# Optimization experiments

Measured on AMD Instinct MI355X. Metric: run time of the kernel, lower is better.

## Reference

```python
import jax, jax.numpy as jnp
import numpy as np

K_KNN = 20
TC = 3  # taylor_channel
N_TERMS = 20  # trivariate polynomial terms up to order 3
CHANNELS = [(6, 32), (32, 64), (64, 128), (128, 256)]


def _knn_indices(xyz, k):
    sq = jnp.sum(xyz * xyz, axis=1)  # B x N
    d2 = sq[:, :, None] + sq[:, None, :] - 2.0 * jnp.einsum('bci,bcj->bij', xyz, xyz)
    _, idx = jax.lax.top_k(-d2, k)
    return idx


def _group(feat, idx):
    # feat: B x C x N, idx: B x N x K -> B x C x N x K
    return jax.vmap(lambda f, i: f[:, i])(feat, idx)


def _taylor_terms(g):
    X, Y, Z = g[:, 0], g[:, 1], g[:, 2]
    one = jnp.ones_like(X)
    terms = [one, X, Y, Z, X * Y, X * Z, Y * Z, X * X, Y * Y, Z * Z,
             X * X * Y, X * X * Z, X * Y * Y, Y * Y * Z, X * Z * Z, Y * Z * Z,
             X * Y * Z, X * X * X, Y * Y * Y, Z * Z * Z]
    return jnp.stack(terms, axis=1)


def _spider_conv(feat, idx, terms, w1, b1, w2, b2):
    # feat: B x C x N; w1: tc x 20; w2: out x (C*tc) x K
    B, C, N = feat.shape
    g = _group(feat, idx)  # B x C x N x K
    taylor = jnp.einsum('btnk,ot->bonk', terms, w1) + b1[None, :, None, None]
    g = (g[:, :, None, :, :] * taylor[:, None, :, :, :]).reshape(B, C * TC, N, g.shape[-1])
    out = jnp.einsum('bcnk,ock->bon', g, w2) + b2[None, :, None]
    return jax.nn.relu(out)


def _forward(pc, params):
    # pc: B x N x 6
    pcT = jnp.transpose(pc, (0, 2, 1))
    xyz = pcT[:, 0:3, :]
    idx = _knn_indices(xyz, K_KNN)  # B x N x K
    grouped_xyz = _group(xyz, idx)
    grouped_pc = grouped_xyz - xyz[:, :, :, None]  # relative coords
    terms = _taylor_terms(grouped_pc)
    feat = pcT
    feats = []
    for l in range(4):
        w1, b1, w2, b2 = params[l]
        feat = _spider_conv(feat, idx, terms, w1, b1, w2, b2)
        feats.append(feat)
    cat = jnp.concatenate(feats, axis=1)
    top2, _ = jax.lax.top_k(cat, 2)  # topk over point dim (last axis)
    return top2.reshape(cat.shape[0], -1)  # B x 960


def setup_inputs() -> dict:
    key = jax.random.key(0)
    keys = jax.random.split(key, 1 + 16)
    B, N = 4, 2048
    inp = {'pc': jax.random.normal(keys[0], (B, N, 6), dtype=jnp.float32)}
    ki = 1
    for l, (cin, cout) in enumerate(CHANNELS):
        inp[f'w1_{l}'] = jax.random.normal(keys[ki], (TC, N_TERMS), dtype=jnp.float32) * 0.1; ki += 1
        inp[f'b1_{l}'] = jax.random.normal(keys[ki], (TC,), dtype=jnp.float32) * 0.01; ki += 1
        inp[f'w2_{l}'] = jax.random.normal(keys[ki], (cout, cin * TC, K_KNN), dtype=jnp.float32) * (1.0 / np.sqrt(cin * TC * K_KNN)); ki += 1
        inp[f'b2_{l}'] = jax.random.normal(keys[ki], (cout,), dtype=jnp.float32) * 0.01; ki += 1
    return inp


def reference(pc, w1_0, b1_0, w2_0, b2_0, w1_1, b1_1, w2_1, b2_1,
              w1_2, b1_2, w2_2, b2_2, w1_3, b1_3, w2_3, b2_3):
    params = [(w1_0, b1_0, w2_0, b2_0), (w1_1, b1_1, w2_1, b2_1),
              (w1_2, b1_2, w2_2, b2_2), (w1_3, b1_3, w2_3, b2_3)]
    return _forward(pc, params)
```

## Files before the change

### kernel.cpp

```cpp
#include <hip/hip_runtime.h>
#include <math.h>

#define BB 4
#define NN 2048
#define KNN 20

typedef _Float16 f16x8 __attribute__((ext_vector_type(8)));
typedef _Float16 f16x4 __attribute__((ext_vector_type(4)));
typedef _Float16 f16x2 __attribute__((ext_vector_type(2)));
typedef float f32x4 __attribute__((ext_vector_type(4)));

#define DPP_STEP(CTRL, RMASK)                                                   \
    {                                                                           \
        unsigned ov = (unsigned)__builtin_amdgcn_update_dpp(                    \
            (int)bv, (int)bv, CTRL, RMASK, 0xf, false);                         \
        unsigned oj = (unsigned)__builtin_amdgcn_update_dpp(                    \
            (int)jj, (int)jj, CTRL, RMASK, 0xf, false);                         \
        bool lt = (ov < bv) || (ov == bv && oj < jj);                           \
        bv = lt ? ov : bv;                                                      \
        jj = lt ? oj : jj;                                                      \
    }

__global__ __launch_bounds__(256) void knn_kernel(const float* __restrict__ pc,
                                                  int* __restrict__ idx_out,
                                                  float* __restrict__ rel_out) {
    __shared__ float sx[NN], sy[NN], sz[NN], sq[NN];
    const int tid = threadIdx.x;
    const int b = blockIdx.x / (NN / 4);
    const int grp = blockIdx.x % (NN / 4);
    for (int p = tid; p < NN; p += 256) {
        float x = pc[(size_t)(b * NN + p) * 6 + 0];
        float y = pc[(size_t)(b * NN + p) * 6 + 1];
        float z = pc[(size_t)(b * NN + p) * 6 + 2];
        sx[p] = x; sy[p] = y; sz[p] = z;
        sq[p] = __fadd_rn(__fadd_rn(__fmul_rn(x, x), __fmul_rn(y, y)), __fmul_rn(z, z));
    }
    __syncthreads();
    const int lane = tid & 63;
    const int i = grp * 4 + (tid >> 6);
    const float xi = sx[i], yi = sy[i], zi = sz[i];
    const float sqi = sq[i];

    unsigned mmr[32];
#pragma unroll
    for (int t = 0; t < 32; ++t) {
        const int j = t * 64 + lane;
        float dot = __fadd_rn(__fadd_rn(__fmul_rn(xi, sx[j]), __fmul_rn(yi, sy[j])),
                              __fmul_rn(zi, sz[j]));
        float d2 = __fsub_rn(__fadd_rn(sqi, sq[j]), __fmul_rn(2.0f, dot));
        unsigned bbits = __float_as_uint(d2);
        mmr[t] = bbits ^ (0x80000000u | (unsigned)((int)bbits >> 31));
    }

    const unsigned UMAX = 0xFFFFFFFFu;
    unsigned mask = 0u;
    unsigned v1, t1, v2, t2;

    auto refill = [&]() {
        v1 = UMAX; t1 = 0u; v2 = UMAX; t2 = 0u;
#pragma unroll
        for (int t = 0; t < 32; ++t) {
            unsigned m = ((mask >> t) & 1u) ? UMAX : mmr[t];
            bool c1 = m < v1;
            bool c2 = m < v2;
            unsigned nv2 = c1 ? v1 : (c2 ? m : v2);
            unsigned nt2 = c1 ? t1 : (c2 ? (unsigned)t : t2);
            v1 = c1 ? m : v1;
            t1 = c1 ? (unsigned)t : t1;
            v2 = nv2; t2 = nt2;
        }
    };
    refill();

    const size_t orow = (size_t)(b * NN + i);
    for (int k = 0; k < KNN; ++k) {
        unsigned bv = v1;
        unsigned jj = (t1 << 6) | (unsigned)lane;
        DPP_STEP(0x111, 0xf)
        DPP_STEP(0x112, 0xf)
        DPP_STEP(0x114, 0xf)
        DPP_STEP(0x118, 0xf)
        DPP_STEP(0x142, 0xa)
        DPP_STEP(0x143, 0xc)
        const unsigned sj = (unsigned)__builtin_amdgcn_readlane((int)jj, 63);
        if (lane == 0) {
            idx_out[orow * KNN + k] = (int)sj;
            size_t ro = (orow * KNN + k) * 3;
            rel_out[ro + 0] = __fsub_rn(sx[sj], xi);
            rel_out[ro + 1] = __fsub_rn(sy[sj], yi);
            rel_out[ro + 2] = __fsub_rn(sz[sj], zi);
        }
        if (k < KNN - 1) {
            bool am = ((sj & 63u) == (unsigned)lane);
            if (am) {
                mask |= (1u << (sj >> 6));
                v1 = v2; t1 = t2; v2 = UMAX;
            }
            if (__ballot(v1 == UMAX) != 0ull) refill();
        }
    }
}

__global__ __launch_bounds__(256) void taylor_all_kernel(
    const float* __restrict__ rel,
    const float* __restrict__ w10, const float* __restrict__ b10, float* __restrict__ ty0,
    const float* __restrict__ w11, const float* __restrict__ b11, float* __restrict__ ty1,
    const float* __restrict__ w12, const float* __restrict__ b12, float* __restrict__ ty2,
    const float* __restrict__ w13, const float* __restrict__ b13, float* __restrict__ ty3) {
    __shared__ float w1s[4][60];
    __shared__ float b1s[4][3];
    const int tid = threadIdx.x;
    if (tid < 240) {
        const float* wp = (tid < 60) ? w10 : (tid < 120) ? w11 : (tid < 180) ? w12 : w13;
        w1s[tid / 60][tid % 60] = wp[tid % 60];
    } else if (tid < 252) {
        int r = tid - 240;
        const float* bp = (r < 3) ? b10 : (r < 6) ? b11 : (r < 9) ? b12 : b13;
        b1s[r / 3][r % 3] = bp[r % 3];
    }
    __syncthreads();
    int t = blockIdx.x * 256 + tid;
    if (t >= BB * NN * KNN) return;
    float X = rel[(size_t)t * 3 + 0], Y = rel[(size_t)t * 3 + 1], Z = rel[(size_t)t * 3 + 2];
    float tm[20];
    tm[0] = 1.f; tm[1] = X; tm[2] = Y; tm[3] = Z;
    tm[4] = X * Y; tm[5] = X * Z; tm[6] = Y * Z;
    tm[7] = X * X; tm[8] = Y * Y; tm[9] = Z * Z;
    tm[10] = X * X * Y; tm[11] = X * X * Z; tm[12] = X * Y * Y; tm[13] = Y * Y * Z;
    tm[14] = X * Z * Z; tm[15] = Y * Z * Z; tm[16] = X * Y * Z;
    tm[17] = X * X * X; tm[18] = Y * Y * Y; tm[19] = Z * Z * Z;
    float* typ[4] = {ty0, ty1, ty2, ty3};
#pragma unroll
    for (int l = 0; l < 4; ++l) {
#pragma unroll
        for (int o = 0; o < 3; ++o) {
            float a = b1s[l][o];
#pragma unroll
            for (int q = 0; q < 20; ++q) a += w1s[l][o * 20 + q] * tm[q];
            typ[l][(size_t)t * 3 + o] = a;
        }
    }
}

struct WsplitArgs {
    const float* w2[4];
    _Float16* wf[4];
    int COUT[4], CIN[4], CPAD[4], OCB[4], KCB[4];
    int cum[4];
};

__global__ __launch_bounds__(256) void wsplit_all_kernel(WsplitArgs a) {
    int e = blockIdx.x * 256 + threadIdx.x;
    if (e >= a.cum[3]) return;
    int l = (e >= a.cum[0]) + (e >= a.cum[1]) + (e >= a.cum[2]);
    int base = l ? a.cum[l - 1] : 0;
    e -= base;
    const int KCB = a.KCB[l], OCB = a.OCB[l], CPAD = a.CPAD[l], CIN = a.CIN[l];
    int i = e & 7;
    int lane = (e >> 3) & 63;
    int fi = e >> 9;
    int kcb = fi % KCB;
    int ocb = (fi / KCB) % OCB;
    int k = fi / (KCB * OCB);
    int oc = ocb * 16 + (lane & 15);
    int kk = kcb * 32 + (lane >> 4) * 8 + i;
    int o = kk / CPAD, c = kk % CPAD;
    float x = 0.f;
    if (o < 3 && c < CIN)
        x = a.w2[l][((size_t)oc * (CIN * 3) + c * 3 + o) * KNN + k];
    a.wf[l][e] = (_Float16)x;
}

template <int CIN, int COUT, int CK3P, int NT, int WM, int WN, int FM, int FN,
          int OCT, int KSPLIT, bool L0S>
__global__ __launch_bounds__(256) void convm_kernel(const float* __restrict__ fin,
                                                    const int* __restrict__ idx,
                                                    const float* __restrict__ tyg,
                                                    const _Float16* __restrict__ wf,
                                                    float* __restrict__ out) {
    constexpr int KR = KNN / KSPLIT;
    constexpr int SR = CK3P + 8;
    constexpr int KCB = CK3P / 32;
    constexpr int OCB = COUT / 16;
    constexpr int OCBLK = WM * FM * 16;
    constexpr int NTL = NN / NT;
    constexpr int TPR = 256 / NT;
    constexpr int CT = L0S ? 6 : (CIN / TPR);
    constexpr int CQ = L0S ? 2 : (CT / 4);
    static_assert(WN * FN * 16 == NT, "n tiling");
    static_assert(OCBLK * OCT == COUT, "oc tiling");
    static_assert(WM * WN == 4, "4 waves");
    static_assert(OCT * KSPLIT == 4 && NTL == 32 && NT == 64, "xcd decode");

    __shared__ _Float16 Bs[NT * SR];
    __shared__ _Float16 tyt[NT][3 * KR];
    __shared__ int idxt[NT][KR];

    const int tid = threadIdx.x;
    const int lane = tid & 63;
    const int wid = tid >> 6;
    const int wm = wid / WN;
    const int wn = wid % WN;
    const int bid = blockIdx.x;
    const int e_ = (bid & 7) >> 1;
    const int oct = e_ / KSPLIT;
    const int ks = e_ % KSPLIT;
    const int hi = ((bid >> 3) << 1) | (bid & 1);
    const int ntl = hi & 31;
    const int b = hi >> 5;
    const int n0 = ntl * NT;
    const int oc0 = oct * OCBLK;
    const int k0 = ks * KR;
    const size_t brow = (size_t)b * NN;

    for (int e = tid; e < NT * KR; e += 256) {
        int n = e / KR, kk = e % KR;
        idxt[n][kk] = idx[(brow + n0 + n) * KNN + k0 + kk];
    }
    for (int e = tid; e < NT * 3 * KR; e += 256) {
        int n = e / (3 * KR), q = e % (3 * KR);
        tyt[n][q] = (_Float16)tyg[((brow + n0 + n) * KNN + k0) * 3 + q];
    }
    __syncthreads();

    const int nrow = tid & 63;
    const int sub = tid >> 6;
    float4 g[CQ];

    auto issue_gather = [&](int kk) {
        if constexpr (L0S) {
            if (tid < 192) {
                int j = idxt[nrow][kk];
                const float* p = fin + (brow + j) * 6;
                g[0] = *reinterpret_cast<const float4*>(p);
                float2 r2 = *reinterpret_cast<const float2*>(p + 4);
                g[1].x = r2.x; g[1].y = r2.y;
            }
        } else {
            int j = idxt[nrow][kk];
            const float* p = fin + (brow + j) * CIN + sub * CT;
#pragma unroll
            for (int q = 0; q < CQ; ++q)
                g[q] = *reinterpret_cast<const float4*>(p + q * 4);
        }
    };
    issue_gather(0);

    f32x4 acc[FM][FN];
#pragma unroll
    for (int fm = 0; fm < FM; ++fm)
#pragma unroll
        for (int fn = 0; fn < FN; ++fn) acc[fm][fn] = (f32x4){0.f, 0.f, 0.f, 0.f};

    auto loadA = [&](int k, int kcb, f16x8* a) {
#pragma unroll
        for (int fm = 0; fm < FM; ++fm) {
            size_t fidx = ((size_t)k * OCB + (oc0 >> 4) + wm * FM + fm) * KCB + kcb;
            a[fm] = *reinterpret_cast<const f16x8*>(&wf[(fidx * 64 + lane) * 8]);
        }
    };
    auto loadB = [&](int kcb, f16x8* bb) {
#pragma unroll
        for (int fn = 0; fn < FN; ++fn) {
            int row = wn * FN * 16 + fn * 16 + (lane & 15);
            bb[fn] = *reinterpret_cast<const f16x8*>(
                &Bs[row * SR + kcb * 32 + (lane >> 4) * 8]);
        }
    };

    for (int kk = 0; kk < KR; ++kk) {
        const int k = k0 + kk;
        __syncthreads();
        if constexpr (L0S) {
            if (tid < 192) {
                _Float16 th = tyt[nrow][kk * 3 + sub];
                f16x2 tb; tb[0] = th; tb[1] = th;
                f16x2 g0, g1, g2;
                g0[0] = (_Float16)g[0].x; g0[1] = (_Float16)g[0].y;
                g1[0] = (_Float16)g[0].z; g1[1] = (_Float16)g[0].w;
                g2[0] = (_Float16)g[1].x; g2[1] = (_Float16)g[1].y;
                f16x2 p0 = g0 * tb, p1 = g1 * tb, p2 = g2 * tb;
                f16x8 hv;
                hv[0] = p0[0]; hv[1] = p0[1]; hv[2] = p1[0]; hv[3] = p1[1];
                hv[4] = p2[0]; hv[5] = p2[1]; hv[6] = (_Float16)0.f; hv[7] = (_Float16)0.f;
                *reinterpret_cast<f16x8*>(&Bs[nrow * SR + sub * 8]) = hv;
                if (sub == 0) {
                    f16x8 z = {};
                    *reinterpret_cast<f16x8*>(&Bs[nrow * SR + 24]) = z;
                }
            }
        } else {
            f16x2 gh[CT / 2];
#pragma unroll
            for (int q = 0; q < CQ; ++q) {
                f16x2 a0, a1;
                a0[0] = (_Float16)g[q].x; a0[1] = (_Float16)g[q].y;
                a1[0] = (_Float16)g[q].z; a1[1] = (_Float16)g[q].w;
                gh[2 * q] = a0; gh[2 * q + 1] = a1;
            }
            _Float16 th0 = tyt[nrow][kk * 3 + 0];
            _Float16 th1 = tyt[nrow][kk * 3 + 1];
            _Float16 th2 = tyt[nrow][kk * 3 + 2];
#pragma unroll
            for (int o = 0; o < 3; ++o) {
                _Float16 th = (o == 0) ? th0 : (o == 1) ? th1 : th2;
                f16x2 tb; tb[0] = th; tb[1] = th;
#pragma unroll
                for (int qp = 0; qp < CT / 8; ++qp) {
                    f16x2 p0 = gh[4 * qp + 0] * tb;
                    f16x2 p1 = gh[4 * qp + 1] * tb;
                    f16x2 p2 = gh[4 * qp + 2] * tb;
                    f16x2 p3 = gh[4 * qp + 3] * tb;
                    f16x8 hv;
                    hv[0] = p0[0]; hv[1] = p0[1]; hv[2] = p1[0]; hv[3] = p1[1];
                    hv[4] = p2[0]; hv[5] = p2[1]; hv[6] = p3[0]; hv[7] = p3[1];
                    *reinterpret_cast<f16x8*>(
                        &Bs[nrow * SR + o * CIN + sub * CT + qp * 8]) = hv;
                }
            }
        }
        __syncthreads();
        if (kk + 1 < KR) issue_gather(kk + 1);
        f16x8 aC[FM], bC[FN], aN[FM], bN[FN];
        loadA(k, 0, aC);
        loadB(0, bC);
#pragma unroll
        for (int kcb = 0; kcb < KCB; ++kcb) {
            if (kcb + 1 < KCB) { loadA(k, kcb + 1, aN); loadB(kcb + 1, bN); }
#pragma unroll
            for (int fm = 0; fm < FM; ++fm)
#pragma unroll
                for (int fn = 0; fn < FN; ++fn)
                    acc[fm][fn] = __builtin_amdgcn_mfma_f32_16x16x32_f16(
                        aC[fm], bC[fn], acc[fm][fn], 0, 0, 0);
            if (kcb + 1 < KCB) {
#pragma unroll
                for (int fm = 0; fm < FM; ++fm) aC[fm] = aN[fm];
#pragma unroll
                for (int fn = 0; fn < FN; ++fn) bC[fn] = bN[fn];
            }
        }
    }
    float* dst = out + (size_t)ks * ((size_t)BB * NN * COUT);
#pragma unroll
    for (int fm = 0; fm < FM; ++fm) {
        const int ocb = oc0 + wm * FM * 16 + fm * 16 + ((lane >> 4) << 2);
#pragma unroll
        for (int fn = 0; fn < FN; ++fn) {
            int n = n0 + wn * FN * 16 + fn * 16 + (lane & 15);
            float4 o4;
            o4.x = acc[fm][fn][0]; o4.y = acc[fm][fn][1];
            o4.z = acc[fm][fn][2]; o4.w = acc[fm][fn][3];
            *reinterpret_cast<float4*>(&dst[(brow + n) * COUT + ocb]) = o4;
        }
    }
}

template <int COUT, int KS>
__global__ __launch_bounds__(256) void combine_kernel(const float* __restrict__ p,
                                                      const float* __restrict__ b2,
                                                      float* __restrict__ out) {
    constexpr size_t TOT = (size_t)BB * NN * COUT;
    size_t i = (size_t)blockIdx.x * 256 + threadIdx.x;
    if (i * 4 >= TOT) return;
    const float4* p4 = reinterpret_cast<const float4*>(p);
    float4 a = p4[i];
#pragma unroll
    for (int s = 1; s < KS; ++s) {
        float4 v = p4[i + s * (TOT / 4)];
        a.x += v.x; a.y += v.y; a.z += v.z; a.w += v.w;
    }
    float4 bb = *reinterpret_cast<const float4*>(&b2[(i * 4) % COUT]);
    float4 r;
    r.x = fmaxf(a.x + bb.x, 0.f); r.y = fmaxf(a.y + bb.y, 0.f);
    r.z = fmaxf(a.z + bb.z, 0.f); r.w = fmaxf(a.w + bb.w, 0.f);
    reinterpret_cast<float4*>(out)[i] = r;
}

__global__ __launch_bounds__(256) void top2_kernel(const float* __restrict__ f1,
                                                   const float* __restrict__ f2,
                                                   const float* __restrict__ f3,
                                                   const float* __restrict__ p3,
                                                   const float* __restrict__ b23,
                                                   float* __restrict__ out) {
    __shared__ float m1s[256], m2s[256];
    const int bid = blockIdx.x;
    const int b = bid / 480;
    const int ch = bid % 480;
    const size_t brow = (size_t)b * NN;
    float m1 = -INFINITY, m2 = -INFINITY;
    if (ch < 224) {
        const float* f; int C, c;
        if (ch < 32)       { f = f1; C = 32;  c = ch; }
        else if (ch < 96)  { f = f2; C = 64;  c = ch - 32; }
        else               { f = f3; C = 128; c = ch - 96; }
        for (int n = threadIdx.x; n < NN; n += 256) {
            float v = f[(brow + n) * C + c];
            if (v > m1) { m2 = m1; m1 = v; }
            else if (v > m2) m2 = v;
        }
    } else {
        const int c = ch - 224;
        const float bc = b23[c];
        constexpr size_t TOT3 = (size_t)BB * NN * 256;
        for (int n = threadIdx.x; n < NN; n += 256) {
            size_t o = (brow + n) * 256 + c;
            float v = fmaxf(p3[o] + p3[TOT3 + o] + bc, 0.f);
            if (v > m1) { m2 = m1; m1 = v; }
            else if (v > m2) m2 = v;
        }
    }
    m1s[threadIdx.x] = m1; m2s[threadIdx.x] = m2;
    __syncthreads();
    for (int s = 128; s > 0; s >>= 1) {
        if (threadIdx.x < s) {
            float a1 = m1s[threadIdx.x], a2 = m2s[threadIdx.x];
            float c1 = m1s[threadIdx.x + s], c2 = m2s[threadIdx.x + s];
            m1s[threadIdx.x] = fmaxf(a1, c1);
            m2s[threadIdx.x] = fmaxf(fminf(a1, c1), fmaxf(a2, c2));
        }
        __syncthreads();
    }
    if (threadIdx.x == 0) {
        out[(size_t)b * 960 + ch * 2 + 0] = m1s[0];
        out[(size_t)b * 960 + ch * 2 + 1] = m2s[0];
    }
}

extern "C" void kernel_launch(void* const* d_in, const int* in_sizes, int n_in,
                              void* d_out, int out_size, void* d_ws, size_t ws_size,
                              hipStream_t stream) {
    const float* pc = (const float*)d_in[0];
    const float *w1[4], *b1[4], *w2[4], *b2[4];
    for (int l = 0; l < 4; ++l) {
        w1[l] = (const float*)d_in[1 + 4 * l];
        b1[l] = (const float*)d_in[2 + 4 * l];
        w2[l] = (const float*)d_in[3 + 4 * l];
        b2[l] = (const float*)d_in[4 + 4 * l];
    }
    char* ws = (char*)d_ws;
    size_t off = 0;
    auto alloc = [&](size_t bytes) -> void* {
        void* p = ws + off;
        off = (off + bytes + 255) & ~(size_t)255;
        return p;
    };
    int* idxb     = (int*)alloc((size_t)BB * NN * KNN * 4);
    float* rel    = (float*)alloc((size_t)BB * NN * KNN * 3 * 4);
    float* ty0    = (float*)alloc((size_t)BB * NN * KNN * 3 * 4);
    float* ty1    = (float*)alloc((size_t)BB * NN * KNN * 3 * 4);
    float* ty2    = (float*)alloc((size_t)BB * NN * KNN * 3 * 4);
    float* ty3    = (float*)alloc((size_t)BB * NN * KNN * 3 * 4);
    const int wtot0 = KNN * 2 * 1 * 512;
    const int wtot1 = KNN * 4 * 3 * 512;
    const int wtot2 = KNN * 8 * 6 * 512;
    const int wtot3 = KNN * 16 * 12 * 512;
    _Float16* wf0 = (_Float16*)alloc((size_t)wtot0 * 2);
    _Float16* wf1 = (_Float16*)alloc((size_t)wtot1 * 2);
    _Float16* wf2 = (_Float16*)alloc((size_t)wtot2 * 2);
    _Float16* wf3 = (_Float16*)alloc((size_t)wtot3 * 2);
    float* f1     = (float*)alloc((size_t)BB * NN * 32 * 4);
    float* f2     = (float*)alloc((size_t)BB * NN * 64 * 4);
    float* f3     = (float*)alloc((size_t)BB * NN * 128 * 4);
    float* pbuf   = (float*)alloc((size_t)4 * BB * NN * 128 * 4);

    knn_kernel<<<BB * NN / 4, 256, 0, stream>>>(pc, idxb, rel);

    taylor_all_kernel<<<(BB * NN * KNN + 255) / 256, 256, 0, stream>>>(
        rel, w1[0], b1[0], ty0, w1[1], b1[1], ty1, w1[2], b1[2], ty2, w1[3], b1[3], ty3);

    WsplitArgs wa;
    wa.w2[0] = w2[0]; wa.w2[1] = w2[1]; wa.w2[2] = w2[2]; wa.w2[3] = w2[3];
    wa.wf[0] = wf0; wa.wf[1] = wf1; wa.wf[2] = wf2; wa.wf[3] = wf3;
    int COUTs[4] = {32, 64, 128, 256}, CINs[4] = {6, 32, 64, 128};
    int CPADs[4] = {8, 32, 64, 128}, OCBs[4] = {2, 4, 8, 16}, KCBs[4] = {1, 3, 6, 12};
    int cum = 0;
    for (int l = 0; l < 4; ++l) {
        wa.COUT[l] = COUTs[l]; wa.CIN[l] = CINs[l]; wa.CPAD[l] = CPADs[l];
        wa.OCB[l] = OCBs[l]; wa.KCB[l] = KCBs[l];
        cum += KNN * OCBs[l] * KCBs[l] * 512;
        wa.cum[l] = cum;
    }
    wsplit_all_kernel<<<(cum + 255) / 256, 256, 0, stream>>>(wa);

    convm_kernel<6, 32, 32, 64, 2, 2, 1, 2, 1, 4, true>
        <<<512, 256, 0, stream>>>(pc, idxb, ty0, wf0, pbuf);
    combine_kernel<32, 4><<<(BB * NN * 32 / 4 + 255) / 256, 256, 0, stream>>>(pbuf, b2[0], f1);

    convm_kernel<32, 64, 96, 64, 4, 1, 1, 4, 1, 4, false>
        <<<512, 256, 0, stream>>>(f1, idxb, ty1, wf1, pbuf);
    combine_kernel<64, 4><<<(BB * NN * 64 / 4 + 255) / 256, 256, 0, stream>>>(pbuf, b2[1], f2);

    convm_kernel<64, 128, 192, 64, 4, 1, 2, 4, 1, 4, false>
        <<<512, 256, 0, stream>>>(f2, idxb, ty2, wf2, pbuf);
    combine_kernel<128, 4><<<(BB * NN * 128 / 4 + 255) / 256, 256, 0, stream>>>(pbuf, b2[2], f3);

    convm_kernel<128, 256, 384, 64, 4, 1, 2, 4, 2, 2, false>
        <<<512, 256, 0, stream>>>(f3, idxb, ty3, wf3, pbuf);

    top2_kernel<<<BB * 480, 256, 0, stream>>>(f1, f2, f3, pbuf, b2[3], (float*)d_out);
}
```

Before: 202.2 us.

## Pack knn points as float4, store taylor in fp16, burst-load conv weights

The knn kernel now packs x,y,z and the squared norm into one float4 per point in shared memory, replacing four separate arrays with a single vector LDS read. The taylor coefficients are written and read as fp16, which halves that intermediate's traffic and drops a convert in the conv kernel. The conv kernel loads all A-weight fragments for a neighbour slot into registers before the inner MFMA loop instead of double-buffering them, and it replaces the XCD-aware block-index decode with a plain linear decode. The register burst raises VGPR pressure and may reduce occupancy, and losing the XCD swizzle may hurt L2 locality.

```diff
diff --git a/kernel.cpp b/kernel.cpp
--- a/kernel.cpp
+++ b/kernel.cpp
@@ -24,7 +24,7 @@
 __global__ __launch_bounds__(256) void knn_kernel(const float* __restrict__ pc,
                                                   int* __restrict__ idx_out,
                                                   float* __restrict__ rel_out) {
-    __shared__ float sx[NN], sy[NN], sz[NN], sq[NN];
+    __shared__ float4 sp[NN];
     const int tid = threadIdx.x;
     const int b = blockIdx.x / (NN / 4);
     const int grp = blockIdx.x % (NN / 4);
@@ -32,22 +32,25 @@
         float x = pc[(size_t)(b * NN + p) * 6 + 0];
         float y = pc[(size_t)(b * NN + p) * 6 + 1];
         float z = pc[(size_t)(b * NN + p) * 6 + 2];
-        sx[p] = x; sy[p] = y; sz[p] = z;
-        sq[p] = __fadd_rn(__fadd_rn(__fmul_rn(x, x), __fmul_rn(y, y)), __fmul_rn(z, z));
+        float4 v;
+        v.x = x; v.y = y; v.z = z;
+        v.w = __fadd_rn(__fadd_rn(__fmul_rn(x, x), __fmul_rn(y, y)), __fmul_rn(z, z));
+        sp[p] = v;
     }
     __syncthreads();
     const int lane = tid & 63;
     const int i = grp * 4 + (tid >> 6);
-    const float xi = sx[i], yi = sy[i], zi = sz[i];
-    const float sqi = sq[i];
+    const float4 pi = sp[i];
+    const float xi = pi.x, yi = pi.y, zi = pi.z, sqi = pi.w;
 
     unsigned mmr[32];
 #pragma unroll
     for (int t = 0; t < 32; ++t) {
         const int j = t * 64 + lane;
-        float dot = __fadd_rn(__fadd_rn(__fmul_rn(xi, sx[j]), __fmul_rn(yi, sy[j])),
-                              __fmul_rn(zi, sz[j]));
-        float d2 = __fsub_rn(__fadd_rn(sqi, sq[j]), __fmul_rn(2.0f, dot));
+        const float4 pj = sp[j];
+        float dot = __fadd_rn(__fadd_rn(__fmul_rn(xi, pj.x), __fmul_rn(yi, pj.y)),
+                              __fmul_rn(zi, pj.z));
+        float d2 = __fsub_rn(__fadd_rn(sqi, pj.w), __fmul_rn(2.0f, dot));
         unsigned bbits = __float_as_uint(d2);
         mmr[t] = bbits ^ (0x80000000u | (unsigned)((int)bbits >> 31));
     }
@@ -85,10 +88,11 @@
         const unsigned sj = (unsigned)__builtin_amdgcn_readlane((int)jj, 63);
         if (lane == 0) {
             idx_out[orow * KNN + k] = (int)sj;
+            const float4 pj = sp[sj];
             size_t ro = (orow * KNN + k) * 3;
-            rel_out[ro + 0] = __fsub_rn(sx[sj], xi);
-            rel_out[ro + 1] = __fsub_rn(sy[sj], yi);
-            rel_out[ro + 2] = __fsub_rn(sz[sj], zi);
+            rel_out[ro + 0] = __fsub_rn(pj.x, xi);
+            rel_out[ro + 1] = __fsub_rn(pj.y, yi);
+            rel_out[ro + 2] = __fsub_rn(pj.z, zi);
         }
         if (k < KNN - 1) {
             bool am = ((sj & 63u) == (unsigned)lane);
@@ -103,10 +107,10 @@
 
 __global__ __launch_bounds__(256) void taylor_all_kernel(
     const float* __restrict__ rel,
-    const float* __restrict__ w10, const float* __restrict__ b10, float* __restrict__ ty0,
-    const float* __restrict__ w11, const float* __restrict__ b11, float* __restrict__ ty1,
-    const float* __restrict__ w12, const float* __restrict__ b12, float* __restrict__ ty2,
-    const float* __restrict__ w13, const float* __restrict__ b13, float* __restrict__ ty3) {
+    const float* __restrict__ w10, const float* __restrict__ b10, _Float16* __restrict__ ty0,
+    const float* __restrict__ w11, const float* __restrict__ b11, _Float16* __restrict__ ty1,
+    const float* __restrict__ w12, const float* __restrict__ b12, _Float16* __restrict__ ty2,
+    const float* __restrict__ w13, const float* __restrict__ b13, _Float16* __restrict__ ty3) {
     __shared__ float w1s[4][60];
     __shared__ float b1s[4][3];
     const int tid = threadIdx.x;
@@ -129,7 +133,7 @@
     tm[10] = X * X * Y; tm[11] = X * X * Z; tm[12] = X * Y * Y; tm[13] = Y * Y * Z;
     tm[14] = X * Z * Z; tm[15] = Y * Z * Z; tm[16] = X * Y * Z;
     tm[17] = X * X * X; tm[18] = Y * Y * Y; tm[19] = Z * Z * Z;
-    float* typ[4] = {ty0, ty1, ty2, ty3};
+    _Float16* typ[4] = {ty0, ty1, ty2, ty3};
 #pragma unroll
     for (int l = 0; l < 4; ++l) {
 #pragma unroll
@@ -137,7 +141,7 @@
             float a = b1s[l][o];
 #pragma unroll
             for (int q = 0; q < 20; ++q) a += w1s[l][o * 20 + q] * tm[q];
-            typ[l][(size_t)t * 3 + o] = a;
+            typ[l][(size_t)t * 3 + o] = (_Float16)a;
         }
     }
 }
@@ -175,7 +179,7 @@
           int OCT, int KSPLIT, bool L0S>
 __global__ __launch_bounds__(256) void convm_kernel(const float* __restrict__ fin,
                                                     const int* __restrict__ idx,
-                                                    const float* __restrict__ tyg,
+                                                    const _Float16* __restrict__ tyg,
                                                     const _Float16* __restrict__ wf,
                                                     float* __restrict__ out) {
     constexpr int KR = KNN / KSPLIT;
@@ -190,7 +194,6 @@
     static_assert(WN * FN * 16 == NT, "n tiling");
     static_assert(OCBLK * OCT == COUT, "oc tiling");
     static_assert(WM * WN == 4, "4 waves");
-    static_assert(OCT * KSPLIT == 4 && NTL == 32 && NT == 64, "xcd decode");
 
     __shared__ _Float16 Bs[NT * SR];
     __shared__ _Float16 tyt[NT][3 * KR];
@@ -201,13 +204,11 @@
     const int wid = tid >> 6;
     const int wm = wid / WN;
     const int wn = wid % WN;
-    const int bid = blockIdx.x;
-    const int e_ = (bid & 7) >> 1;
-    const int oct = e_ / KSPLIT;
-    const int ks = e_ % KSPLIT;
-    const int hi = ((bid >> 3) << 1) | (bid & 1);
-    const int ntl = hi & 31;
-    const int b = hi >> 5;
+    int t = blockIdx.x;
+    const int ks = t % KSPLIT; t /= KSPLIT;
+    const int oct = t % OCT;   t /= OCT;
+    const int ntl = t % NTL;   t /= NTL;
+    const int b = t;
     const int n0 = ntl * NT;
     const int oc0 = oct * OCBLK;
     const int k0 = ks * KR;
@@ -219,7 +220,7 @@
     }
     for (int e = tid; e < NT * 3 * KR; e += 256) {
         int n = e / (3 * KR), q = e % (3 * KR);
-        tyt[n][q] = (_Float16)tyg[((brow + n0 + n) * KNN + k0) * 3 + q];
+        tyt[n][q] = tyg[((brow + n0 + n) * KNN + k0) * 3 + q];
     }
     __syncthreads();
 
@@ -252,24 +253,21 @@
 #pragma unroll
         for (int fn = 0; fn < FN; ++fn) acc[fm][fn] = (f32x4){0.f, 0.f, 0.f, 0.f};
 
-    auto loadA = [&](int k, int kcb, f16x8* a) {
-#pragma unroll
-        for (int fm = 0; fm < FM; ++fm) {
-            size_t fidx = ((size_t)k * OCB + (oc0 >> 4) + wm * FM + fm) * KCB + kcb;
-            a[fm] = *reinterpret_cast<const f16x8*>(&wf[(fidx * 64 + lane) * 8]);
-        }
-    };
-    auto loadB = [&](int kcb, f16x8* bb) {
-#pragma unroll
-        for (int fn = 0; fn < FN; ++fn) {
-            int row = wn * FN * 16 + fn * 16 + (lane & 15);
-            bb[fn] = *reinterpret_cast<const f16x8*>(
-                &Bs[row * SR + kcb * 32 + (lane >> 4) * 8]);
-        }
+    f16x8 areg[FM * KCB];
+    auto loadA_burst = [&](int k) {
+#pragma unroll
+        for (int fm = 0; fm < FM; ++fm)
+#pragma unroll
+            for (int kcb = 0; kcb < KCB; ++kcb) {
+                size_t fidx = ((size_t)k * OCB + (oc0 >> 4) + wm * FM + fm) * KCB + kcb;
+                areg[fm * KCB + kcb] =
+                    *reinterpret_cast<const f16x8*>(&wf[(fidx * 64 + lane) * 8]);
+            }
     };
 
     for (int kk = 0; kk < KR; ++kk) {
         const int k = k0 + kk;
+        loadA_burst(k);
         __syncthreads();
         if constexpr (L0S) {
             if (tid < 192) {
@@ -321,24 +319,21 @@
         }
         __syncthreads();
         if (kk + 1 < KR) issue_gather(kk + 1);
-        f16x8 aC[FM], bC[FN], aN[FM], bN[FN];
-        loadA(k, 0, aC);
-        loadB(0, bC);
 #pragma unroll
         for (int kcb = 0; kcb < KCB; ++kcb) {
-            if (kcb + 1 < KCB) { loadA(k, kcb + 1, aN); loadB(kcb + 1, bN); }
+            f16x8 bf[FN];
+#pragma unroll
+            for (int fn = 0; fn < FN; ++fn) {
+                int row = wn * FN * 16 + fn * 16 + (lane & 15);
+                bf[fn] = *reinterpret_cast<const f16x8*>(
+                    &Bs[row * SR + kcb * 32 + (lane >> 4) * 8]);
+            }
 #pragma unroll
             for (int fm = 0; fm < FM; ++fm)
 #pragma unroll
                 for (int fn = 0; fn < FN; ++fn)
                     acc[fm][fn] = __builtin_amdgcn_mfma_f32_16x16x32_f16(
-                        aC[fm], bC[fn], acc[fm][fn], 0, 0, 0);
-            if (kcb + 1 < KCB) {
-#pragma unroll
-                for (int fm = 0; fm < FM; ++fm) aC[fm] = aN[fm];
-#pragma unroll
-                for (int fn = 0; fn < FN; ++fn) bC[fn] = bN[fn];
-            }
+                        areg[fm * KCB + kcb], bf[fn], acc[fm][fn], 0, 0, 0);
         }
     }
     float* dst = out + (size_t)ks * ((size_t)BB * NN * COUT);
@@ -445,12 +440,12 @@
         off = (off + bytes + 255) & ~(size_t)255;
         return p;
     };
-    int* idxb     = (int*)alloc((size_t)BB * NN * KNN * 4);
-    float* rel    = (float*)alloc((size_t)BB * NN * KNN * 3 * 4);
-    float* ty0    = (float*)alloc((size_t)BB * NN * KNN * 3 * 4);
-    float* ty1    = (float*)alloc((size_t)BB * NN * KNN * 3 * 4);
-    float* ty2    = (float*)alloc((size_t)BB * NN * KNN * 3 * 4);
-    float* ty3    = (float*)alloc((size_t)BB * NN * KNN * 3 * 4);
+    int* idxb      = (int*)alloc((size_t)BB * NN * KNN * 4);
+    float* rel     = (float*)alloc((size_t)BB * NN * KNN * 3 * 4);
+    _Float16* ty0  = (_Float16*)alloc((size_t)BB * NN * KNN * 3 * 2);
+    _Float16* ty1  = (_Float16*)alloc((size_t)BB * NN * KNN * 3 * 2);
+    _Float16* ty2  = (_Float16*)alloc((size_t)BB * NN * KNN * 3 * 2);
+    _Float16* ty3  = (_Float16*)alloc((size_t)BB * NN * KNN * 3 * 2);
     const int wtot0 = KNN * 2 * 1 * 512;
     const int wtot1 = KNN * 4 * 3 * 512;
     const int wtot2 = KNN * 8 * 6 * 512;
```

After: 191.0 us. 5.5% less time.
